# Kernel optimization log

Hardware: AMD Instinct MI355X
Metric: run time of the kernel (lower is better)

Reference implementation:

```python
import jax, jax.numpy as jnp
import numpy as np

B, C, H, W = 4, 512, 64, 64
NUM_HEADS = 4
NUM_GROUPS = 32
EPS = 1e-5


def setup_inputs() -> dict:
    key = jax.random.key(0)
    ks = jax.random.split(key, 7)
    x = jax.random.normal(ks[0], (B, C, H, W), dtype=jnp.float32)
    gn_gamma = jnp.ones((C,), dtype=jnp.float32)
    gn_beta = jnp.zeros((C,), dtype=jnp.float32)
    # Conv2d 1x1 weights stored as [out_ch, in_ch]
    qkv_w = jax.random.normal(ks[1], (3 * C, C), dtype=jnp.float32) * (C ** -0.5)
    qkv_b = jax.random.normal(ks[2], (3 * C,), dtype=jnp.float32) * 0.01
    out_w = jax.random.normal(ks[3], (C, C), dtype=jnp.float32) * (C ** -0.5)
    out_b = jax.random.normal(ks[4], (C,), dtype=jnp.float32) * 0.01
    return {"x": x, "gn_gamma": gn_gamma, "gn_beta": gn_beta,
            "qkv_w": qkv_w, "qkv_b": qkv_b, "out_w": out_w, "out_b": out_b}


def _group_norm(x, gamma, beta):
    b, c, h, w = x.shape
    xg = x.reshape(b, NUM_GROUPS, c // NUM_GROUPS, h, w)
    mean = xg.mean(axis=(2, 3, 4), keepdims=True)
    var = xg.var(axis=(2, 3, 4), keepdims=True)
    xg = (xg - mean) * jax.lax.rsqrt(var + EPS)
    x = xg.reshape(b, c, h, w)
    return x * gamma[None, :, None, None] + beta[None, :, None, None]


def reference(x, gn_gamma, gn_beta, qkv_w, qkv_b, out_w, out_b):
    residual = x
    b, c, h, w = x.shape
    hc = c // NUM_HEADS
    n = h * w
    xn = _group_norm(x, gn_gamma, gn_beta)
    # 1x1 conv == channel matmul: [B, 3C, H, W]
    qkv = jnp.einsum('oc,bchw->bohw', qkv_w, xn) + qkv_b[None, :, None, None]
    q, k, v = jnp.split(qkv, 3, axis=1)
    # [B, C, H, W] -> [B, heads, N, hc]
    def to_heads(t):
        return t.reshape(b, NUM_HEADS, hc, n).transpose(0, 1, 3, 2)
    q, k, v = to_heads(q), to_heads(k), to_heads(v)
    scale = hc ** -0.5
    attn = jnp.einsum('bhnd,bhmd->bhnm', q, k) * scale
    attn = jax.nn.softmax(attn, axis=-1)
    o = jnp.einsum('bhnm,bhmd->bhnd', attn, v)
    # back to [B, C, H, W]
    o = o.transpose(0, 1, 3, 2).reshape(b, c, h, w)
    o = o + residual
    out = jnp.einsum('oc,bchw->bohw', out_w, o) + out_b[None, :, None, None]
    return out
```

## Files before the change

kernel.cpp:

```cpp
#include <hip/hip_runtime.h>
#include <math.h>

constexpr int BB = 4, CH = 512, NN = 4096, NHEADS = 4, NGROUPS = 32, HCH = 128;
constexpr float EPS = 1e-5f;
constexpr float SCALE = 0.08838834764831845f;
constexpr float LOG2E = 1.4426950408889634f;
constexpr float QSCALE = SCALE * LOG2E;
constexpr float THR = 11.541560327111707f;

typedef short bf16x8 __attribute__((ext_vector_type(8)));
typedef float f32x4 __attribute__((ext_vector_type(4)));
typedef float f32x16 __attribute__((ext_vector_type(16)));

__device__ __forceinline__ float bf2f(unsigned short u) {
    unsigned int x = ((unsigned int)u) << 16;
    float f; __builtin_memcpy(&f, &x, 4); return f;
}
__device__ __forceinline__ unsigned short f2bf(float f) {
    unsigned int x; __builtin_memcpy(&x, &f, 4);
    x += 0x7fff + ((x >> 16) & 1);
    return (unsigned short)(x >> 16);
}
__device__ __forceinline__ unsigned int cvtpk(float lo, float hi) {
    unsigned int r;
    asm("v_cvt_pk_bf16_f32 %0, %1, %2" : "=v"(r) : "v"(lo), "v"(hi));
    return r;
}
__device__ __forceinline__ float fexp2(float x) {
    float r; asm("v_exp_f32 %0, %1" : "=v"(r) : "v"(x)); return r;
}

__device__ __forceinline__ void gld16(const void* g, void* l) {
    __builtin_amdgcn_global_load_lds(
        (const __attribute__((address_space(1))) void*)g,
        (__attribute__((address_space(3))) void*)l, 16, 0, 0);
}

__global__ __launch_bounds__(256) void prep_kernel(
    const float* __restrict__ qkv_w, const float* __restrict__ out_w,
    const float* __restrict__ x,
    unsigned short* __restrict__ wq_bf, unsigned short* __restrict__ wo_bf,
    float* __restrict__ stats)
{
    int bid = blockIdx.x;
    if (bid < 1024) {
        int i4 = bid * 256 + threadIdx.x;
        if (i4 < 196608) {
            float4 w = ((const float4*)qkv_w)[i4];
            int row = i4 >> 7;
            float sc = (row < 512) ? QSCALE : 1.0f;
            ushort4 o = { f2bf(w.x * sc), f2bf(w.y * sc), f2bf(w.z * sc), f2bf(w.w * sc) };
            *(ushort4*)&wq_bf[(size_t)i4 * 4] = o;
        } else {
            int j4 = i4 - 196608;
            float4 w = ((const float4*)out_w)[j4];
            ushort4 o = { f2bf(w.x), f2bf(w.y), f2bf(w.z), f2bf(w.w) };
            *(ushort4*)&wo_bf[(size_t)j4 * 4] = o;
        }
        return;
    }
    const int CPG = CH / NGROUPS;
    int gb = bid - 1024;
    int bg = gb >> 2, part = gb & 3;
    int b = bg / NGROUPS, g = bg % NGROUPS;
    const size_t base = ((size_t)b * CH + (size_t)g * CPG) * NN
                      + (size_t)part * (CPG * NN / 4);
    const int total4 = CPG * NN / 16;
    int tid = threadIdx.x;

    const float4* x4 = (const float4*)(x + base);
    float sum = 0.f, sumsq = 0.f;
    for (int i = tid; i < total4; i += 256) {
        float4 v = x4[i];
        sum   += v.x + v.y + v.z + v.w;
        sumsq += v.x*v.x + v.y*v.y + v.z*v.z + v.w*v.w;
    }
    for (int off = 32; off > 0; off >>= 1) {
        sum   += __shfl_down(sum, off);
        sumsq += __shfl_down(sumsq, off);
    }
    __shared__ float s_sum[4], s_sq[4];
    int wid = tid >> 6, lane = tid & 63;
    if (lane == 0) { s_sum[wid] = sum; s_sq[wid] = sumsq; }
    __syncthreads();
    if (tid == 0) {
        float ts = 0.f, tq = 0.f;
        for (int i = 0; i < 4; i++) { ts += s_sum[i]; tq += s_sq[i]; }
        atomicAdd(&stats[bg * 2 + 0], ts);
        atomicAdd(&stats[bg * 2 + 1], tq);
    }
}

__global__ __launch_bounds__(256) void t1_kernel(
    const float* __restrict__ x, const float2* __restrict__ stats,
    const float* __restrict__ gamma, const float* __restrict__ beta,
    unsigned short* __restrict__ xnT, unsigned short* __restrict__ xT)
{
    __shared__ alignas(16) short Tn[64 * 80];
    __shared__ alignas(16) short Tr[64 * 80];
    int n0 = blockIdx.x * 64, c0 = blockIdx.y * 64, b = blockIdx.z;
    int tid = threadIdx.x;
    const float inv = 1.0f / 65536.0f;

    #pragma unroll
    for (int i = 0; i < 4; ++i) {
        int idx = tid + i * 256; int cl = idx >> 4, nq = idx & 15;
        int c = c0 + cl;
        float2 st = stats[b * NGROUPS + (c >> 4)];
        float mean = st.x * inv;
        float var  = st.y * inv - mean * mean;
        float rstd = rsqrtf(var + EPS);
        float gm = gamma[c], bt = beta[c];
        float4 f = *(const float4*)&x[((size_t)(b * CH + c)) * NN + n0 + nq * 4];
        float e0 = f.x, e1 = f.y, e2 = f.z, e3 = f.w;
        int cs = cl ^ ((nq & 7) << 3);
        Tr[(nq * 4 + 0) * 80 + cs] = (short)f2bf(e0);
        Tr[(nq * 4 + 1) * 80 + cs] = (short)f2bf(e1);
        Tr[(nq * 4 + 2) * 80 + cs] = (short)f2bf(e2);
        Tr[(nq * 4 + 3) * 80 + cs] = (short)f2bf(e3);
        Tn[(nq * 4 + 0) * 80 + cs] = (short)f2bf((e0 - mean) * rstd * gm + bt);
        Tn[(nq * 4 + 1) * 80 + cs] = (short)f2bf((e1 - mean) * rstd * gm + bt);
        Tn[(nq * 4 + 2) * 80 + cs] = (short)f2bf((e2 - mean) * rstd * gm + bt);
        Tn[(nq * 4 + 3) * 80 + cs] = (short)f2bf((e3 - mean) * rstd * gm + bt);
    }
    __syncthreads();
    #pragma unroll
    for (int i = 0; i < 2; ++i) {
        int idx = tid + i * 256; int n = idx >> 3, ck = idx & 7;
        int cs8 = (ck * 8) ^ (((n >> 2) & 7) << 3);
        size_t gidx = ((size_t)(b * NN + n0 + n)) * CH + c0 + ck * 8;
        *(uint4*)&xnT[gidx] = *(uint4*)&Tn[n * 80 + cs8];
        *(uint4*)&xT[gidx]  = *(uint4*)&Tr[n * 80 + cs8];
    }
}

template<int MODE>
__global__ __launch_bounds__(256) void gemm_kernel(
    const unsigned short* __restrict__ A,
    const unsigned short* __restrict__ Bt,
    const float* __restrict__ bias,
    unsigned short* __restrict__ qT, unsigned short* __restrict__ kT,
    unsigned short* __restrict__ v, float* __restrict__ out)
{
    __shared__ alignas(16) short smem[2][2][128 * 64];
    short* Es = (short*)smem;
    float* Ef = (float*)smem;

    constexpr int GY = (MODE == 0) ? 12 : 4;
    int lin = blockIdx.x + 32 * (blockIdx.y + GY * blockIdx.z);
    constexpr int CPX = 32 * GY * 4 / 8;
    int wg = (lin & 7) * CPX + (lin >> 3);
    const int n0 = (wg % 32) * 128;
    const int m0 = ((wg / 32) % GY) * 128;
    const int b  = wg / (32 * GY);

    const int tid = threadIdx.x;
    const int wid = tid >> 6, l = tid & 63, lr = l & 15, lk = l >> 4;
    const int wm = (wid & 1) * 64, wn = (wid >> 1) * 64;
    const unsigned short* Bb = Bt + (size_t)b * NN * CH;

    int rr[4], LL[4], ch[4];
    #pragma unroll
    for (int i = 0; i < 4; ++i) {
        ch[i] = (wid * 4 + i) * 1024;
        int li = ch[i] + l * 16;
        int r = li >> 7, s = (li >> 4) & 7;
        rr[i] = r; LL[i] = s ^ (r & 7);
    }

    #define GSTAGE(buf, k0) do {                                                   \
        _Pragma("unroll")                                                          \
        for (int i = 0; i < 4; ++i) {                                              \
            gld16(&A [((size_t)(m0 + rr[i])) * CH + (k0) + LL[i] * 8],             \
                  (char*)&smem[buf][0][0] + ch[i]);                                \
            gld16(&Bb[((size_t)(n0 + rr[i])) * CH + (k0) + LL[i] * 8],             \
                  (char*)&smem[buf][1][0] + ch[i]);                                \
        }                                                                          \
    } while (0)

    f32x4 acc[4][4];
    #pragma unroll
    for (int i = 0; i < 4; ++i)
        #pragma unroll
        for (int j = 0; j < 4; ++j) acc[i][j] = (f32x4){0.f, 0.f, 0.f, 0.f};

    GSTAGE(0, 0);
    __syncthreads();

    int cur = 0;
    for (int ks = 0; ks < 8; ++ks) {
        if (ks < 7) GSTAGE(cur ^ 1, (ks + 1) * 64);
        const char* As = (const char*)&smem[cur][0][0];
        const char* Bs = (const char*)&smem[cur][1][0];
        #pragma unroll
        for (int kh = 0; kh < 2; ++kh) {
            const int sw = ((kh * 4 + lk) ^ (lr & 7)) << 4;
            bf16x8 af[4], bfr[4];
            #pragma unroll
            for (int t = 0; t < 4; ++t) {
                af[t]  = *(const bf16x8*)(As + (wm + t * 16 + lr) * 128 + sw);
                bfr[t] = *(const bf16x8*)(Bs + (wn + t * 16 + lr) * 128 + sw);
            }
            #pragma unroll
            for (int mt = 0; mt < 4; ++mt)
                #pragma unroll
                for (int nt = 0; nt < 4; ++nt)
                    acc[mt][nt] = __builtin_amdgcn_mfma_f32_16x16x32_bf16(
                        af[mt], bfr[nt], acc[mt][nt], 0, 0, 0);
        }
        __syncthreads();
        cur ^= 1;
    }
    #undef GSTAGE

    if (MODE == 0) {
        const bool isV = (m0 >= 1024);
        #pragma unroll
        for (int mt = 0; mt < 4; ++mt) {
            int mbase = m0 + wm + mt * 16 + lk * 4;
            int ml = wm + mt * 16 + lk * 4;
            float bsc = (m0 < 512) ? QSCALE : 1.0f;
            #pragma unroll
            for (int nt = 0; nt < 4; ++nt) {
                int nl = wn + nt * 16 + lr;
                f32x4 vv = acc[mt][nt];
                if (!isV) {
                    ushort4 o;
                    o.x = f2bf(vv[0] + bias[mbase + 0] * bsc);
                    o.y = f2bf(vv[1] + bias[mbase + 1] * bsc);
                    o.z = f2bf(vv[2] + bias[mbase + 2] * bsc);
                    o.w = f2bf(vv[3] + bias[mbase + 3] * bsc);
                    *(ushort4*)&Es[nl * 132 + ml] = o;
                } else {
                    #pragma unroll
                    for (int j = 0; j < 4; ++j)
                        Es[(ml + j) * 132 + nl] = (short)f2bf(vv[j] + bias[mbase + j]);
                }
            }
        }
        __syncthreads();
        int r16 = tid >> 4, c16 = tid & 15;
        if (!isV) {
            unsigned short* dst;
            if (m0 < 512) dst = qT + (((size_t)(b * 4 + (m0 >> 7))) * NN + n0) * 128;
            else          dst = kT + (((size_t)(b * 4 + ((m0 - 512) >> 7))) * NN + n0) * 128;
            #pragma unroll
            for (int p = 0; p < 8; ++p) {
                int nl = p * 16 + r16;
                uint4 w = *(const uint4*)&Es[nl * 132 + c16 * 8];
                *(uint4*)&dst[(size_t)nl * 128 + c16 * 8] = w;
            }
        } else {
            unsigned short* dst = v + ((size_t)(b * 512 + (m0 - 1024)) * NN) + n0;
            #pragma unroll
            for (int p = 0; p < 8; ++p) {
                int ml = p * 16 + r16;
                uint4 w = *(const uint4*)&Es[ml * 132 + c16 * 8];
                *(uint4*)&dst[(size_t)ml * NN + c16 * 8] = w;
            }
        }
    } else {
        for (int half = 0; half < 2; ++half) {
            __syncthreads();
            if ((wn >> 6) == half) {
                #pragma unroll
                for (int mt = 0; mt < 4; ++mt) {
                    int ml = wm + mt * 16 + lk * 4;
                    int mbase = m0 + ml;
                    #pragma unroll
                    for (int nt = 0; nt < 4; ++nt) {
                        int nl = nt * 16 + lr;
                        f32x4 vv = acc[mt][nt];
                        #pragma unroll
                        for (int j = 0; j < 4; ++j)
                            Ef[(ml + j) * 66 + nl] = vv[j] + bias[mbase + j];
                    }
                }
            }
            __syncthreads();
            #pragma unroll
            for (int i = 0; i < 8; ++i) {
                int idx = tid + i * 256;
                int r = idx >> 4, c4 = idx & 15;
                float4 w = *(const float4*)&Ef[r * 66 + c4 * 4];
                *(float4*)&out[((size_t)(b * CH + m0 + r)) * NN + n0 + half * 64 + c4 * 4] = w;
            }
        }
    }
}

__global__ __launch_bounds__(256, 2) void attn_kernel(
    const unsigned short* __restrict__ qT,
    const unsigned short* __restrict__ kT,
    const unsigned short* __restrict__ vg,
    const unsigned short* __restrict__ xT,
    unsigned short* __restrict__ aoT)
{
    __shared__ alignas(16) short Ks[2][64 * 128];
    __shared__ alignas(16) short Vs[2][64 * 128];

    int lin_id = blockIdx.x + 32 * (blockIdx.y + 4 * blockIdx.z);
    int wg = (lin_id & 7) * 64 + (lin_id >> 3);
    const int n0 = (wg & 31) * 128;
    const int h  = (wg >> 5) & 3;
    const int b  = wg >> 7;

    const int bh = b * 4 + h;
    const int tid = threadIdx.x, wid = tid >> 6, l = tid & 63;
    const int lq = l & 31, hi = l >> 5;
    const int wq0 = wid * 32;
    const int swz4 = (l & 15) << 4;
    const unsigned short* Qg = qT + (size_t)bh * NN * 128;
    const unsigned short* Kg = kT + (size_t)bh * NN * 128;
    const unsigned short* Vg = vg + (size_t)bh * 128 * NN;

    int kr[4], kc[4], vdd[4], vcc[4], ch[4];
    #pragma unroll
    for (int i = 0; i < 4; ++i) {
        ch[i] = (wid * 4 + i) * 1024;
        int li = ch[i] + l * 16;
        int r = li >> 8, s = (li >> 4) & 15;
        int L = s ^ (r & 15);
        kr[i] = r; kc[i] = L;
        vdd[i] = r + 64 * (L >> 3);
        vcc[i] = L & 7;
    }

    #define STAGE(buf, m0k) do {                                                   \
        _Pragma("unroll")                                                          \
        for (int i = 0; i < 4; ++i) {                                              \
            gld16(&Kg[(size_t)((m0k) + kr[i]) * 128 + kc[i] * 8],                  \
                  (char*)&Ks[buf][0] + ch[i]);                                     \
            gld16(&Vg[(size_t)vdd[i] * NN + (m0k) + vcc[i] * 8],                   \
                  (char*)&Vs[buf][0] + ch[i]);                                     \
        }                                                                          \
    } while (0)

    STAGE(0, 0);

    bf16x8 qr[8];
    #pragma unroll
    for (int dk = 0; dk < 8; ++dk)
        qr[dk] = *(const bf16x8*)&Qg[((size_t)(n0 + wq0 + lq)) * 128 + dk * 16 + hi * 8];

    f32x16 ov[4];
    #pragma unroll
    for (int dt = 0; dt < 4; ++dt)
        #pragma unroll
        for (int r = 0; r < 16; ++r) ov[dt][r] = 0.f;
    float mrun = -1e30f, lrun = 0.f;

    __syncthreads();

    int cur = 0;
    for (int t = 0; t < 64; ++t) {
        if (t < 63) STAGE(cur ^ 1, (t + 1) * 64);

        const char* Kc = (const char*)&Ks[cur][0];
        const char* Vc = (const char*)&Vs[cur][0];

        f32x16 s0, s1;
        #pragma unroll
        for (int r = 0; r < 16; ++r) { s0[r] = 0.f; s1[r] = 0.f; }
        __builtin_amdgcn_s_setprio(1);
        #pragma unroll
        for (int dk = 0; dk < 8; ++dk) {
            bf16x8 k0 = *(const bf16x8*)(Kc + (lq)      * 256 + ((dk * 32 + hi * 16) ^ swz4));
            bf16x8 k1 = *(const bf16x8*)(Kc + (32 + lq) * 256 + ((dk * 32 + hi * 16) ^ swz4));
            s0 = __builtin_amdgcn_mfma_f32_32x32x16_bf16(k0, qr[dk], s0, 0, 0, 0);
            s1 = __builtin_amdgcn_mfma_f32_32x32x16_bf16(k1, qr[dk], s1, 0, 0, 0);
        }
        __builtin_amdgcn_s_setprio(0);

        float m8[8];
        #pragma unroll
        for (int r = 0; r < 8; ++r)
            m8[r] = fmaxf(fmaxf(s0[r], s0[r + 8]), fmaxf(s1[r], s1[r + 8]));
        float t0 = fmaxf(fmaxf(m8[0], m8[1]), m8[2]);
        float t1_ = fmaxf(fmaxf(m8[3], m8[4]), m8[5]);
        float t2 = fmaxf(fmaxf(m8[6], m8[7]), t0);
        float pm = fmaxf(t1_, t2);
        pm = fmaxf(pm, __shfl_xor(pm, 32));

        int defer = (pm - mrun) <= THR;
        if (!__all(defer)) {
            float mnew = fmaxf(mrun, pm);
            float corr = fexp2(mrun - mnew);
            lrun *= corr; mrun = mnew;
            #pragma unroll
            for (int dt = 0; dt < 4; ++dt)
                #pragma unroll
                for (int r = 0; r < 16; ++r) ov[dt][r] *= corr;
        }
        float ps = 0.f;
        #pragma unroll
        for (int r = 0; r < 16; ++r) { float e = fexp2(s0[r] - mrun); s0[r] = e; ps += e; }
        #pragma unroll
        for (int r = 0; r < 16; ++r) { float e = fexp2(s1[r] - mrun); s1[r] = e; ps += e; }
        ps += __shfl_xor(ps, 32);
        lrun += ps;

        unsigned int u0[8], u1[8];
        #pragma unroll
        for (int m = 0; m < 8; ++m) {
            u0[m] = cvtpk(s0[2 * m], s0[2 * m + 1]);
            u1[m] = cvtpk(s1[2 * m], s1[2 * m + 1]);
        }
        bf16x8 pf[4];
        #pragma unroll
        for (int kt = 0; kt < 2; ++kt)
            #pragma unroll
            for (int hh = 0; hh < 2; ++hh) {
                const unsigned int* u = kt ? u1 : u0;
                unsigned int w0 = u[4*hh + 0], w2 = u[4*hh + 2];
                unsigned int w1 = u[4*hh + 1], w3 = u[4*hh + 3];
                asm("v_permlane32_swap_b32 %0, %1" : "+v"(w0), "+v"(w2));
                asm("v_permlane32_swap_b32 %0, %1" : "+v"(w1), "+v"(w3));
                unsigned int w[4] = { w0, w1, w2, w3 };
                bf16x8 p; __builtin_memcpy(&p, w, 16);
                pf[kt * 2 + hh] = p;
            }

        __builtin_amdgcn_s_setprio(1);
        #pragma unroll
        for (int dt = 0; dt < 4; ++dt)
            #pragma unroll
            for (int kt2 = 0; kt2 < 4; ++kt2) {
                bf16x8 vf = *(const bf16x8*)(Vc + ((dt & 1) * 32 + lq) * 256 +
                                             ((((dt >> 1) * 8 + kt2 * 2 + hi) << 4) ^ swz4));
                ov[dt] = __builtin_amdgcn_mfma_f32_32x32x16_bf16(vf, pf[kt2], ov[dt], 0, 0, 0);
            }
        __builtin_amdgcn_s_setprio(0);

        __syncthreads();
        cur ^= 1;
    }
    #undef STAGE

    float linv = 1.0f / lrun;
    const int n = n0 + wq0 + lq;
    #pragma unroll
    for (int dt = 0; dt < 4; ++dt)
        #pragma unroll
        for (int m = 0; m < 4; ++m) {
            int d = dt * 32 + m * 8 + hi * 4;
            size_t gidx = ((size_t)(b * NN + n)) * CH + h * 128 + d;
            unsigned short xv[4];
            *(ushort4*)xv = *(const ushort4*)&xT[gidx];
            unsigned int w0 = cvtpk(ov[dt][4*m + 0] * linv + bf2f(xv[0]),
                                    ov[dt][4*m + 1] * linv + bf2f(xv[1]));
            unsigned int w1 = cvtpk(ov[dt][4*m + 2] * linv + bf2f(xv[2]),
                                    ov[dt][4*m + 3] * linv + bf2f(xv[3]));
            unsigned long long wv = (unsigned long long)w0 |
                                    ((unsigned long long)w1 << 32);
            *(unsigned long long*)&aoT[gidx] = wv;
        }
}

extern "C" void kernel_launch(void* const* d_in, const int* in_sizes, int n_in,
                              void* d_out, int out_size, void* d_ws, size_t ws_size,
                              hipStream_t stream) {
    const float* x      = (const float*)d_in[0];
    const float* gamma  = (const float*)d_in[1];
    const float* beta   = (const float*)d_in[2];
    const float* qkv_w  = (const float*)d_in[3];
    const float* qkv_b  = (const float*)d_in[4];
    const float* out_w  = (const float*)d_in[5];
    const float* out_b  = (const float*)d_in[6];
    float* out = (float*)d_out;

    char* ws = (char*)d_ws;
    const size_t SZ = (size_t)BB * CH * NN * 2;
    unsigned short* xnT   = (unsigned short*)(ws);
    unsigned short* xT    = (unsigned short*)(ws + SZ);
    unsigned short* qT    = (unsigned short*)(ws + 2 * SZ);
    unsigned short* kT    = (unsigned short*)(ws + 3 * SZ);
    unsigned short* vbuf  = (unsigned short*)(ws + 4 * SZ);
    unsigned short* aoT   = (unsigned short*)(ws + 5 * SZ);
    unsigned short* wq_bf = (unsigned short*)(ws + 6 * SZ);
    unsigned short* wo_bf = (unsigned short*)(ws + 6 * SZ + (size_t)1536 * 512 * 2);
    float* stats = (float*)(ws + 6 * SZ + (size_t)2048 * 512 * 2);

    hipMemsetAsync(stats, 0, 256 * sizeof(float), stream);
    prep_kernel<<<dim3(1536), 256, 0, stream>>>(qkv_w, out_w, x, wq_bf, wo_bf, stats);
    t1_kernel<<<dim3(NN / 64, CH / 64, BB), 256, 0, stream>>>(
        x, (const float2*)stats, gamma, beta, xnT, xT);
    gemm_kernel<0><<<dim3(NN / 128, 1536 / 128, BB), 256, 0, stream>>>(
        wq_bf, xnT, qkv_b, qT, kT, vbuf, nullptr);
    attn_kernel<<<dim3(NN / 128, NHEADS, BB), 256, 0, stream>>>(qT, kT, vbuf, xT, aoT);
    gemm_kernel<1><<<dim3(NN / 128, CH / 128, BB), 256, 0, stream>>>(
        wo_bf, aoT, out_b, nullptr, nullptr, nullptr, out);
}
```

Baseline: 250.9 us.

## Store K in MFMA-fragment layout and load directly into registers

The QKV projection now writes K in a pre-swizzled fragment order matching the MFMA operand layout. The attention kernel drops the K shared-memory buffer and each wave loads its K fragments straight from global memory into registers, prefetching the next tile after the QK MFMAs. This removes the LDS staging and LDS reads for K and halves shared memory use. The cost is 16 extra vector registers per lane, with every wave redundantly loading the same K tile from global/L2, which may raise register pressure and L2 traffic.

New measurement: 275.0 us. +9.6%, slower.

```diff
diff --git a/kernel.cpp b/kernel.cpp
--- a/kernel.cpp
+++ b/kernel.cpp
@@ -241,14 +241,28 @@
         __syncthreads();
         int r16 = tid >> 4, c16 = tid & 15;
         if (!isV) {
-            unsigned short* dst;
-            if (m0 < 512) dst = qT + (((size_t)(b * 4 + (m0 >> 7))) * NN + n0) * 128;
-            else          dst = kT + (((size_t)(b * 4 + ((m0 - 512) >> 7))) * NN + n0) * 128;
-            #pragma unroll
-            for (int p = 0; p < 8; ++p) {
-                int nl = p * 16 + r16;
-                uint4 w = *(const uint4*)&Es[nl * 132 + c16 * 8];
-                *(uint4*)&dst[(size_t)nl * 128 + c16 * 8] = w;
+            if (m0 < 512) {
+                unsigned short* dst = qT + (((size_t)(b * 4 + (m0 >> 7))) * NN + n0) * 128;
+                #pragma unroll
+                for (int p = 0; p < 8; ++p) {
+                    int nl = p * 16 + r16;
+                    uint4 w = *(const uint4*)&Es[nl * 132 + c16 * 8];
+                    *(uint4*)&dst[(size_t)nl * 128 + c16 * 8] = w;
+                }
+            } else {
+                unsigned short* dst = kT + (size_t)(b * 4 + ((m0 - 512) >> 7)) * NN * 128;
+                #pragma unroll
+                for (int p = 0; p < 8; ++p) {
+                    int f = p * 256 + tid;
+                    int flq = f & 31, fhi = (f >> 5) & 1, fdk = (f >> 6) & 7;
+                    int fs = (f >> 9) & 1, ftl = f >> 10;
+                    int nl = ftl * 64 + fs * 32 + flq;
+                    int d0 = fdk * 16 + fhi * 8;
+                    uint4 w = *(const uint4*)&Es[nl * 132 + d0];
+                    size_t fo = ((((size_t)(n0 >> 6) + ftl) * 2 + fs) * 8 + fdk) * 64
+                              + fhi * 32 + flq;
+                    *(uint4*)&dst[fo * 8] = w;
+                }
             }
         } else {
             unsigned short* dst = v + ((size_t)(b * 512 + (m0 - 1024)) * NN) + n0;
@@ -291,12 +305,11 @@
 
 __global__ __launch_bounds__(256, 2) void attn_kernel(
     const unsigned short* __restrict__ qT,
-    const unsigned short* __restrict__ kT,
+    const unsigned short* __restrict__ kF,
     const unsigned short* __restrict__ vg,
     const unsigned short* __restrict__ xT,
     unsigned short* __restrict__ aoT)
 {
-    __shared__ alignas(16) short Ks[2][64 * 128];
     __shared__ alignas(16) short Vs[2][64 * 128];
 
     int lin_id = blockIdx.x + 32 * (blockIdx.y + 4 * blockIdx.z);
@@ -311,32 +324,39 @@
     const int wq0 = wid * 32;
     const int swz4 = (l & 15) << 4;
     const unsigned short* Qg = qT + (size_t)bh * NN * 128;
-    const unsigned short* Kg = kT + (size_t)bh * NN * 128;
+    const unsigned short* Kf = kF + (size_t)bh * NN * 128;
     const unsigned short* Vg = vg + (size_t)bh * 128 * NN;
 
-    int kr[4], kc[4], vdd[4], vcc[4], ch[4];
+    int vdd[4], vcc[4], ch[4];
     #pragma unroll
     for (int i = 0; i < 4; ++i) {
         ch[i] = (wid * 4 + i) * 1024;
         int li = ch[i] + l * 16;
         int r = li >> 8, s = (li >> 4) & 15;
         int L = s ^ (r & 15);
-        kr[i] = r; kc[i] = L;
         vdd[i] = r + 64 * (L >> 3);
         vcc[i] = L & 7;
     }
 
     #define STAGE(buf, m0k) do {                                                   \
         _Pragma("unroll")                                                          \
-        for (int i = 0; i < 4; ++i) {                                              \
-            gld16(&Kg[(size_t)((m0k) + kr[i]) * 128 + kc[i] * 8],                  \
-                  (char*)&Ks[buf][0] + ch[i]);                                     \
+        for (int i = 0; i < 4; ++i)                                                \
             gld16(&Vg[(size_t)vdd[i] * NN + (m0k) + vcc[i] * 8],                   \
                   (char*)&Vs[buf][0] + ch[i]);                                     \
-        }                                                                          \
     } while (0)
 
+    bf16x8 kreg[16];
+    #define KLOAD(t) do {                                                          \
+        _Pragma("unroll")                                                          \
+        for (int ss = 0; ss < 2; ++ss)                                             \
+            _Pragma("unroll")                                                      \
+            for (int dk = 0; dk < 8; ++dk)                                         \
+                kreg[ss * 8 + dk] = *(const bf16x8*)&Kf[                           \
+                    (((((size_t)(t) * 2 + ss) * 8 + dk) << 6) + l) * 8];           \
+    } while (0)
+
     STAGE(0, 0);
+    KLOAD(0);
 
     bf16x8 qr[8];
     #pragma unroll
@@ -356,7 +376,6 @@
     for (int t = 0; t < 64; ++t) {
         if (t < 63) STAGE(cur ^ 1, (t + 1) * 64);
 
-        const char* Kc = (const char*)&Ks[cur][0];
         const char* Vc = (const char*)&Vs[cur][0];
 
         f32x16 s0, s1;
@@ -365,12 +384,12 @@
         __builtin_amdgcn_s_setprio(1);
         #pragma unroll
         for (int dk = 0; dk < 8; ++dk) {
-            bf16x8 k0 = *(const bf16x8*)(Kc + (lq)      * 256 + ((dk * 32 + hi * 16) ^ swz4));
-            bf16x8 k1 = *(const bf16x8*)(Kc + (32 + lq) * 256 + ((dk * 32 + hi * 16) ^ swz4));
-            s0 = __builtin_amdgcn_mfma_f32_32x32x16_bf16(k0, qr[dk], s0, 0, 0, 0);
-            s1 = __builtin_amdgcn_mfma_f32_32x32x16_bf16(k1, qr[dk], s1, 0, 0, 0);
+            s0 = __builtin_amdgcn_mfma_f32_32x32x16_bf16(kreg[dk],     qr[dk], s0, 0, 0, 0);
+            s1 = __builtin_amdgcn_mfma_f32_32x32x16_bf16(kreg[8 + dk], qr[dk], s1, 0, 0, 0);
         }
         __builtin_amdgcn_s_setprio(0);
+
+        if (t < 63) KLOAD(t + 1);
 
         float m8[8];
         #pragma unroll
@@ -436,6 +455,7 @@
         cur ^= 1;
     }
     #undef STAGE
+    #undef KLOAD
 
     float linv = 1.0f / lrun;
     const int n = n0 + wq0 + lq;
```
